# Kernel tuning notes

Hardware: AMD Instinct MI355X
Metric: run time of the kernel (lower is better)

Reference implementation:

```python
import jax, jax.numpy as jnp
import numpy as np

NUM_STATES = 16
NUM_CHAINS = 8
NUM_NODES = 5000
NUM_ITERS = 100


def setup_inputs() -> dict:
    key = jax.random.key(0)
    k1, k2, k3, k4 = jax.random.split(key, 4)
    return {
        "unnormalized_state_init": jax.random.normal(k1, (NUM_STATES,), dtype=jnp.float32),
        "unnormalized_chain_weights": jax.random.normal(k2, (1, NUM_NODES, NUM_CHAINS), dtype=jnp.float32),
        "unnormalized_emission_matrix": jax.random.normal(k3, (NUM_STATES, NUM_NODES), dtype=jnp.float32),
        "unnormalized_transition_matrix": jax.random.normal(k4, (NUM_STATES, NUM_STATES), dtype=jnp.float32),
    }


def reference(unnormalized_state_init, unnormalized_chain_weights,
              unnormalized_emission_matrix, unnormalized_transition_matrix):
    T = NUM_ITERS
    # log_transform_params: row-stochastic normalizations in log space
    log_state_init = jax.nn.log_softmax(unnormalized_state_init)                    # (S,)
    log_chain_weights = jax.nn.log_softmax(unnormalized_chain_weights, axis=-1)     # (1,N,C)
    log_emission = jax.nn.log_softmax(unnormalized_emission_matrix, axis=1)         # (S,N)
    log_transition = jax.nn.log_softmax(unnormalized_transition_matrix, axis=1)     # (S,S), rows P(next|prev)

    # log_weights: (S,N,C) = log P(node|state) + log P(chain|node,state)
    log_weights = log_emission[:, :, None] + log_chain_weights

    # HMM forward recursion on hidden-state marginals: h_t[j] = logsumexp_i(h_{t-1}[i] + logT[i,j])
    def step(h, _):
        h_new = jax.scipy.special.logsumexp(h[:, None] + log_transition, axis=0)
        return h_new, h_new

    _, hs = jax.lax.scan(step, log_state_init, None, length=T - 1)
    log_hidden_state_probs = jnp.concatenate([log_state_init[None], hs], axis=0)    # (T,S)

    # (T,S,N,C): broadcast hidden-state marginal into node/chain weights
    log_observed_state_probs_ = log_weights[None] + log_hidden_state_probs[:, :, None, None]

    # logsumexp over states (axis 1) then chains (axis -1) == joint logsumexp over axes (1,3)
    log_observed_state_probs = jax.scipy.special.logsumexp(log_observed_state_probs_, axis=(1, 3))  # (T,N)

    # permute(0,1,3,2): (T,S,C,N)
    log_observed_state_probs_perm = jnp.transpose(log_observed_state_probs_, (0, 1, 3, 2))

    return (log_observed_state_probs, log_observed_state_probs_perm, log_hidden_state_probs)
```

## Files before the change

### kernel.cpp

```cpp
#include <hip/hip_runtime.h>
#include <math.h>
#include <stdint.h>

#define S 16
#define C 8
#define N 5000
#define T 100
#define N4 1250

typedef float f32x4 __attribute__((ext_vector_type(4)));

__global__ __launch_bounds__(256) void prep_kernel(const float* __restrict__ u_init,
                                                   const float* __restrict__ u_cw,
                                                   const float* __restrict__ u_e,
                                                   const float* __restrict__ u_T,
                                                   float* __restrict__ ws_le,
                                                   float* __restrict__ ws_lcw,
                                                   float* __restrict__ ws_h,
                                                   float* __restrict__ out_h) {
    const int b = blockIdx.x;
    const int tid = threadIdx.x;

    if (b < 16) {
        const float* row = u_e + b * N;
        __shared__ float red[256];
        float m = -INFINITY;
        for (int n = tid; n < N; n += 256) m = fmaxf(m, row[n]);
        red[tid] = m;
        __syncthreads();
        for (int o = 128; o > 0; o >>= 1) {
            if (tid < o) red[tid] = fmaxf(red[tid], red[tid + o]);
            __syncthreads();
        }
        m = red[0];
        __syncthreads();
        float sum = 0.f;
        for (int n = tid; n < N; n += 256) sum += expf(row[n] - m);
        red[tid] = sum;
        __syncthreads();
        for (int o = 128; o > 0; o >>= 1) {
            if (tid < o) red[tid] += red[tid + o];
            __syncthreads();
        }
        const float lse = m + logf(red[0]);
        for (int n = tid; n < N; n += 256) ws_le[b * N + n] = row[n] - lse;
    } else if (b < 36) {
        const int n = (b - 16) * 256 + tid;
        if (n < N) {
            float v[C];
            float m = -INFINITY;
            for (int c = 0; c < C; ++c) {
                v[c] = u_cw[n * C + c];
                m = fmaxf(m, v[c]);
            }
            float s = 0.f;
            for (int c = 0; c < C; ++c) s += expf(v[c] - m);
            const float lse = m + logf(s);
            for (int c = 0; c < C; ++c) ws_lcw[n * C + c] = v[c] - lse;
        }
    } else {
        if (tid < S) {
            const int j = tid;
            float m = -INFINITY;
            for (int i = 0; i < S; ++i) m = fmaxf(m, u_init[i]);
            float ssum = 0.f;
            for (int i = 0; i < S; ++i) ssum += expf(u_init[i] - m);
            const float lse0 = m + logf(ssum);
            const float h0 = u_init[j] - lse0;
            out_h[j] = h0;
            ws_h[j] = h0;
            float mr = -INFINITY;
            for (int k = 0; k < S; ++k) mr = fmaxf(mr, u_T[j * S + k]);
            float sr = 0.f;
            for (int k = 0; k < S; ++k) sr += expf(u_T[j * S + k] - mr);
            const float lse_row = mr + logf(sr);
            float texp[S];
            #pragma unroll
            for (int i = 0; i < S; ++i) {
                const float lse_i = __shfl(lse_row, i, 64);
                texp[i] = expf(u_T[i * S + j] - lse_i);
            }
            float p = expf(h0);
            for (int t = 1; t < T; ++t) {
                float pn = 0.f;
                #pragma unroll
                for (int i = 0; i < S; ++i) {
                    pn = fmaf(__shfl(p, i, 64), texp[i], pn);
                }
                p = pn;
                const float hv = logf(p);
                out_h[t * S + j] = hv;
                ws_h[t * S + j] = hv;
            }
        }
    }
}

__global__ __launch_bounds__(256) void main_kernel(const float* __restrict__ ws_le,
                                                   const float* __restrict__ ws_lcw,
                                                   const float* __restrict__ ws_h,
                                                   float* __restrict__ out0,
                                                   float* __restrict__ out_perm) {
    const int t = blockIdx.y;
    const int i = blockIdx.x * 256 + threadIdx.x;

    __shared__ float h[S];
    if (threadIdx.x < S) h[threadIdx.x] = ws_h[t * S + threadIdx.x];
    __syncthreads();
    if (i >= N4) return;

    float lc[C][4];
    const f32x4* __restrict__ lcw4 = (const f32x4*)ws_lcw;
    #pragma unroll
    for (int j = 0; j < 8; ++j) {
        const f32x4 v = lcw4[8 * i + j];
        const int nl = j >> 1;
        const int cb = (j & 1) * 4;
        lc[cb + 0][nl] = v.x;
        lc[cb + 1][nl] = v.y;
        lc[cb + 2][nl] = v.z;
        lc[cb + 3][nl] = v.w;
    }

    const f32x4* __restrict__ le4 = (const f32x4*)ws_le;
    f32x4* __restrict__ outp4 = (f32x4*)out_perm + (size_t)t * (S * C * N4);

    float sx = 0.f, sy = 0.f, sz = 0.f, sw = 0.f;

    #pragma unroll
    for (int s = 0; s < S; ++s) {
        const f32x4 e = le4[s * N4 + i];
        const float hs = h[s];
        f32x4 a;
        a.x = e.x + hs;
        a.y = e.y + hs;
        a.z = e.z + hs;
        a.w = e.w + hs;
        const int base = s * C * N4 + i;
        #pragma unroll
        for (int c = 0; c < C; ++c) {
            f32x4 w;
            w.x = a.x + lc[c][0];
            w.y = a.y + lc[c][1];
            w.z = a.z + lc[c][2];
            w.w = a.w + lc[c][3];
            __builtin_nontemporal_store(w, outp4 + base + c * N4);
        }
        sx += expf(a.x);
        sy += expf(a.y);
        sz += expf(a.z);
        sw += expf(a.w);
    }

    f32x4 r;
    r.x = logf(sx);
    r.y = logf(sy);
    r.z = logf(sz);
    r.w = logf(sw);
    __builtin_nontemporal_store(r, (f32x4*)out0 + (size_t)t * N4 + i);
}

extern "C" void kernel_launch(void* const* d_in, const int* in_sizes, int n_in,
                              void* d_out, int out_size, void* d_ws, size_t ws_size,
                              hipStream_t stream) {
    const float* u_init = (const float*)d_in[0];
    const float* u_cw   = (const float*)d_in[1];
    const float* u_e    = (const float*)d_in[2];
    const float* u_T    = (const float*)d_in[3];

    float* out = (float*)d_out;
    float* out0     = out;
    float* out_perm = out + (size_t)T * N;
    float* out_h    = out + (size_t)T * N + (size_t)T * S * C * N;

    float* ws  = (float*)d_ws;
    float* ws_h   = ws;
    float* ws_le  = ws + 1600;
    float* ws_lcw = ws + 1600 + 80000;

    prep_kernel<<<37, 256, 0, stream>>>(u_init, u_cw, u_e, u_T, ws_le, ws_lcw, ws_h, out_h);
    main_kernel<<<dim3(5, T), 256, 0, stream>>>(ws_le, ws_lcw, ws_h, out0, out_perm);
}
```

Measured before the change: 306.8 us.

## Split main kernel into per-state write blocks and separate logsumexp blocks

Restructures the main kernel so each block handles one (t, state) slice of the permuted output, looping over chains and nodes, while an extra block per t computes the logsumexp output. Chain weights are stored transposed (C,N) so per-chain reads are contiguous. This raises the block count to expose more parallelism for the large write-bound output, at the cost of re-reading emission rows and dropping nontemporal stores.

```diff
diff --git a/kernel.cpp b/kernel.cpp
--- a/kernel.cpp
+++ b/kernel.cpp
@@ -15,7 +15,7 @@
                                                    const float* __restrict__ u_e,
                                                    const float* __restrict__ u_T,
                                                    float* __restrict__ ws_le,
-                                                   float* __restrict__ ws_lcw,
+                                                   float* __restrict__ ws_lcwT,
                                                    float* __restrict__ ws_h,
                                                    float* __restrict__ out_h) {
     const int b = blockIdx.x;
@@ -56,7 +56,7 @@
             float s = 0.f;
             for (int c = 0; c < C; ++c) s += expf(v[c] - m);
             const float lse = m + logf(s);
-            for (int c = 0; c < C; ++c) ws_lcw[n * C + c] = v[c] - lse;
+            for (int c = 0; c < C; ++c) ws_lcwT[c * N + n] = v[c] - lse;
         }
     } else {
         if (tid < S) {
@@ -97,67 +97,63 @@
 }
 
 __global__ __launch_bounds__(256) void main_kernel(const float* __restrict__ ws_le,
-                                                   const float* __restrict__ ws_lcw,
+                                                   const float* __restrict__ ws_lcwT,
                                                    const float* __restrict__ ws_h,
                                                    float* __restrict__ out0,
                                                    float* __restrict__ out_perm) {
     const int t = blockIdx.y;
-    const int i = blockIdx.x * 256 + threadIdx.x;
+    const int bx = blockIdx.x;
+    const int tid = threadIdx.x;
 
-    __shared__ float h[S];
-    if (threadIdx.x < S) h[threadIdx.x] = ws_h[t * S + threadIdx.x];
-    __syncthreads();
-    if (i >= N4) return;
+    if (bx < S) {
+        const int s = bx;
+        const float hs = ws_h[t * S + s];
+        const f32x4* __restrict__ le4 = (const f32x4*)ws_le + s * N4;
+        const f32x4* __restrict__ lc4 = (const f32x4*)ws_lcwT;
+        f32x4* __restrict__ out4 = (f32x4*)out_perm + (size_t)(t * S + s) * (C * N4);
 
-    float lc[C][4];
-    const f32x4* __restrict__ lcw4 = (const f32x4*)ws_lcw;
-    #pragma unroll
-    for (int j = 0; j < 8; ++j) {
-        const f32x4 v = lcw4[8 * i + j];
-        const int nl = j >> 1;
-        const int cb = (j & 1) * 4;
-        lc[cb + 0][nl] = v.x;
-        lc[cb + 1][nl] = v.y;
-        lc[cb + 2][nl] = v.z;
-        lc[cb + 3][nl] = v.w;
+        for (int c = 0; c < C; ++c) {
+            for (int base = 0; base < N4; base += 256) {
+                const int n4 = base + tid;
+                if (n4 < N4) {
+                    const f32x4 e = le4[n4];
+                    const f32x4 w = lc4[c * N4 + n4];
+                    f32x4 r;
+                    r.x = e.x + hs + w.x;
+                    r.y = e.y + hs + w.y;
+                    r.z = e.z + hs + w.z;
+                    r.w = e.w + hs + w.w;
+                    out4[c * N4 + n4] = r;
+                }
+            }
+        }
+    } else {
+        __shared__ float h[S];
+        if (tid < S) h[tid] = ws_h[t * S + tid];
+        __syncthreads();
+        const f32x4* __restrict__ le4 = (const f32x4*)ws_le;
+        for (int base = 0; base < N4; base += 256) {
+            const int n4 = base + tid;
+            if (n4 < N4) {
+                float sx = 0.f, sy = 0.f, sz = 0.f, sw = 0.f;
+                #pragma unroll
+                for (int s = 0; s < S; ++s) {
+                    const f32x4 e = le4[s * N4 + n4];
+                    const float hv = h[s];
+                    sx += expf(e.x + hv);
+                    sy += expf(e.y + hv);
+                    sz += expf(e.z + hv);
+                    sw += expf(e.w + hv);
+                }
+                f32x4 r;
+                r.x = logf(sx);
+                r.y = logf(sy);
+                r.z = logf(sz);
+                r.w = logf(sw);
+                ((f32x4*)out0)[(size_t)t * N4 + n4] = r;
+            }
+        }
     }
-
-    const f32x4* __restrict__ le4 = (const f32x4*)ws_le;
-    f32x4* __restrict__ outp4 = (f32x4*)out_perm + (size_t)t * (S * C * N4);
-
-    float sx = 0.f, sy = 0.f, sz = 0.f, sw = 0.f;
-
-    #pragma unroll
-    for (int s = 0; s < S; ++s) {
-        const f32x4 e = le4[s * N4 + i];
-        const float hs = h[s];
-        f32x4 a;
-        a.x = e.x + hs;
-        a.y = e.y + hs;
-        a.z = e.z + hs;
-        a.w = e.w + hs;
-        const int base = s * C * N4 + i;
-        #pragma unroll
-        for (int c = 0; c < C; ++c) {
-            f32x4 w;
-            w.x = a.x + lc[c][0];
-            w.y = a.y + lc[c][1];
-            w.z = a.z + lc[c][2];
-            w.w = a.w + lc[c][3];
-            __builtin_nontemporal_store(w, outp4 + base + c * N4);
-        }
-        sx += expf(a.x);
-        sy += expf(a.y);
-        sz += expf(a.z);
-        sw += expf(a.w);
-    }
-
-    f32x4 r;
-    r.x = logf(sx);
-    r.y = logf(sy);
-    r.z = logf(sz);
-    r.w = logf(sw);
-    __builtin_nontemporal_store(r, (f32x4*)out0 + (size_t)t * N4 + i);
 }
 
 extern "C" void kernel_launch(void* const* d_in, const int* in_sizes, int n_in,
@@ -174,10 +170,10 @@
     float* out_h    = out + (size_t)T * N + (size_t)T * S * C * N;
 
     float* ws  = (float*)d_ws;
-    float* ws_h   = ws;
-    float* ws_le  = ws + 1600;
-    float* ws_lcw = ws + 1600 + 80000;
+    float* ws_h    = ws;
+    float* ws_le   = ws + 1600;
+    float* ws_lcwT = ws + 1600 + 80000;
 
-    prep_kernel<<<37, 256, 0, stream>>>(u_init, u_cw, u_e, u_T, ws_le, ws_lcw, ws_h, out_h);
-    main_kernel<<<dim3(5, T), 256, 0, stream>>>(ws_le, ws_lcw, ws_h, out0, out_perm);
+    prep_kernel<<<37, 256, 0, stream>>>(u_init, u_cw, u_e, u_T, ws_le, ws_lcwT, ws_h, out_h);
+    main_kernel<<<dim3(S + 1, T), 256, 0, stream>>>(ws_le, ws_lcwT, ws_h, out0, out_perm);
 }
```

After: 286.2 us (median of 2 runs). 1.07x faster.
